# Kernel optimization log

Hardware: AMD Instinct MI355X
Metric: run time of the kernel (lower is better)

Reference implementation:

```python
import jax, jax.numpy as jnp
import numpy as np

INPUT_DIM = 1024
OUTPUT_DIM = 1000
DEPTH = 10
LAMBDA_REG = 1e-3
N_INTERNAL = 2 ** DEPTH - 1
N_LEAF = 2 ** DEPTH
BATCH = 16384


def setup_inputs() -> dict:
    key = jax.random.key(0)
    k1, k2, k3 = jax.random.split(key, 3)
    X = jax.random.normal(k1, (BATCH, INPUT_DIM), dtype=jnp.float32)
    # torch nn.Linear weight layout: [out_features, in_features]; scaled to keep
    # sigmoid routing probs away from 0/1 saturation (log-reg term).
    W_internal = jax.random.normal(k2, (N_INTERNAL, INPUT_DIM + 1), dtype=jnp.float32) * 0.02
    W_leaf = jax.random.normal(k3, (OUTPUT_DIM, N_LEAF), dtype=jnp.float32) * 0.02
    return {"X": X, "W_internal": W_internal, "W_leaf": W_leaf}


def _tree_paths(X, W_internal):
    B = X.shape[0]
    Xb = jnp.concatenate([jnp.ones((B, 1), X.dtype), X], axis=1)  # [B, D+1]
    logits = jax.nn.sigmoid(Xb @ W_internal.T)                    # [B, N_int]
    routing = jnp.stack([logits, 1.0 - logits], axis=2)           # [B, N_int, 2]
    path = jnp.ones((B, 1), X.dtype)
    reg = jnp.float32(0.0)
    start = 0
    for layer in range(DEPTH):
        n = 2 ** layer
        lp = routing[:, start:start + n, :].reshape(B, 2 * n)     # next_paths [B, 2n]
        path = jnp.repeat(path, 2, axis=1) * lp                   # new path probs [B, 2n]
        # Faithful to source: parent_idx = node_idx // 2 indexes the UPDATED path probs.
        parent = jnp.repeat(path[:, :n], 2, axis=1)               # [B, 2n]
        num = jnp.sum(lp * parent, axis=0)                        # [2n]
        den = jnp.sum(parent, axis=0) + 1e-8                      # [2n]
        alpha = num / den
        factor = LAMBDA_REG * 2.0 ** (-layer)
        reg = reg + factor * jnp.sum(-0.5 * (jnp.log(alpha) + jnp.log(1.0 - alpha)))
        start += n
    return path, reg  # path: [B, 2^DEPTH]


def reference(X, W_internal, W_leaf):
    path_probs, reg = _tree_paths(X, W_internal)
    predictions = path_probs @ W_leaf.T   # [B, output_dim]
    return predictions, reg
```

## Files before the change

### kernel.cpp

```cpp
#include <hip/hip_runtime.h>
#include <hip/hip_bf16.h>

#define B_ROWS 16384
#define K_DIM  1024
#define N_INT  1023
#define N_OUT  1000

using s8vec = __attribute__((ext_vector_type(8))) short;
using f32x4 = __attribute__((ext_vector_type(4))) float;

static const size_t OFF_XB   = 0;
static const size_t OFF_W1   = OFF_XB   + 33554432;
static const size_t OFF_BIAS = OFF_W1   + 2097152;
static const size_t OFF_PROB = OFF_BIAS + 4096;
static const size_t OFF_PATH = OFF_PROB + 33554432;
static const size_t OFF_W2   = OFF_PATH + 33554432;
static const size_t OFF_SG   = OFF_W2   + 2097152;

__device__ __forceinline__ float b2f(ushort u) {
  return __uint_as_float(((unsigned)u) << 16);
}
__device__ __forceinline__ float blo(unsigned u) { return __uint_as_float(u << 16); }
__device__ __forceinline__ float bhi(unsigned u) { return __uint_as_float(u & 0xffff0000u); }
__device__ __forceinline__ ushort f2b(float f) {
  unsigned u = __float_as_uint(f);
  u = u + 0x7FFFu + ((u >> 16) & 1u);
  return (ushort)(u >> 16);
}

__device__ __forceinline__ void load_lds16(const ushort* g, ushort* l) {
  __builtin_amdgcn_global_load_lds((const __attribute__((address_space(1))) void*)g,
                                   (__attribute__((address_space(3))) void*)l,
                                   16, 0, 0);
}

__global__ __launch_bounds__(256) void cvt_all(const float4* __restrict__ X,
                                               ushort4* __restrict__ O,
                                               const float* __restrict__ Wi,
                                               const float* __restrict__ Wl,
                                               ushort* __restrict__ W1,
                                               ushort* __restrict__ W2,
                                               float* __restrict__ bias) {
  const int b = blockIdx.x;
  if (b < 16384) {
    const int i = b * 256 + threadIdx.x;
    const float4 v = X[i];
    ushort4 o;
    o.x = f2b(v.x); o.y = f2b(v.y); o.z = f2b(v.z); o.w = f2b(v.w);
    O[i] = o;
  } else {
    const int idx = (b - 16384) * 256 + threadIdx.x;
    if (idx < (1 << 20)) {
      const int n = idx >> 10, k = idx & 1023;
      const float v = (n < N_INT) ? Wi[n * 1025 + 1 + k] : 0.f;
      W1[idx] = f2b(v);
      if (k == 0) bias[n] = (n < N_INT) ? Wi[n * 1025] : 0.f;
    } else {
      const int j = idx - (1 << 20);
      const int n = j >> 10, k = j & 1023;
      const float v = (n < N_OUT) ? Wl[n * 1024 + k] : 0.f;
      W2[j] = f2b(v);
    }
  }
}

template <int MODE>
__global__ __launch_bounds__(256, 4) void gemm_bt(const ushort* __restrict__ A,
                                                  const ushort* __restrict__ Bm,
                                                  const float* __restrict__ bias,
                                                  void* __restrict__ outp) {
  __shared__ ushort As[2][4096];
  __shared__ ushort Bs[2][4096];
  const int tid = threadIdx.x;
  const int bm = blockIdx.x, bn = blockIdx.y;
  const int lane = tid & 63, wv = tid >> 6;
  const int wm = wv >> 1, wn = wv & 1;
  const int m16 = lane & 15, q = lane >> 4;
  const int qs = q ^ ((m16 >> 1) & 3);

  const int r0 = tid >> 2;
  const int qsw = (tid & 3) ^ ((r0 >> 1) & 3);
  const ushort* aG = A  + (size_t)(bm * 128 + r0) * 1024 + qsw * 8;
  const ushort* bG = Bm + (size_t)(bn * 128 + r0) * 1024 + qsw * 8;

  f32x4 acc[4][4] = {};

#define STAGE(buf, kk) do {                                   \
    load_lds16(aG + (kk), As[buf] + wv * 512);                \
    load_lds16(aG + 65536 + (kk), As[buf] + 2048 + wv * 512); \
    load_lds16(bG + (kk), Bs[buf] + wv * 512);                \
    load_lds16(bG + 65536 + (kk), Bs[buf] + 2048 + wv * 512); \
  } while (0)

#define COMPUTE(cur) do {                                                        \
    s8vec af[4], bfv[4];                                                         \
    _Pragma("unroll")                                                            \
    for (int i = 0; i < 4; ++i)                                                  \
      af[i] = *(const s8vec*)(As[cur] + (wm * 64 + i * 16 + m16) * 32 + qs * 8); \
    _Pragma("unroll")                                                            \
    for (int j = 0; j < 4; ++j)                                                  \
      bfv[j] = *(const s8vec*)(Bs[cur] + (wn * 64 + j * 16 + m16) * 32 + qs * 8);\
    _Pragma("unroll")                                                            \
    for (int i = 0; i < 4; ++i)                                                  \
      _Pragma("unroll")                                                          \
      for (int j = 0; j < 4; ++j)                                                \
        acc[i][j] = __builtin_amdgcn_mfma_f32_16x16x32_bf16(af[i], bfv[j],       \
                                                            acc[i][j], 0, 0, 0);\
  } while (0)

  STAGE(0, 0);
#pragma unroll 1
  for (int k0 = 0; k0 < 992; k0 += 32) {
    const int cur = (k0 >> 5) & 1;
    STAGE(cur ^ 1, k0 + 32);
    asm volatile("s_waitcnt vmcnt(4)\n\ts_barrier" ::: "memory");
    COMPUTE(cur);
    asm volatile("s_barrier" ::: "memory");
  }
  asm volatile("s_waitcnt vmcnt(0)\n\ts_barrier" ::: "memory");
  COMPUTE(1);
#undef STAGE
#undef COMPUTE

  if (MODE == 0) {
    ushort* P = (ushort*)outp;
#pragma unroll
    for (int i = 0; i < 4; ++i)
#pragma unroll
      for (int r = 0; r < 4; ++r) {
        const int gr = bm * 128 + wm * 64 + i * 16 + q * 4 + r;
#pragma unroll
        for (int j = 0; j < 4; ++j) {
          const int gc = bn * 128 + wn * 64 + j * 16 + m16;
          const float z = acc[i][j][r] + bias[gc];
          const float p = 1.f / (1.f + expf(-z));
          if (gc < N_INT) P[(size_t)gr * 1024 + gc + 1] = f2b(p);
        }
      }
  } else {
    float* O = (float*)outp;
#pragma unroll
    for (int i = 0; i < 4; ++i)
#pragma unroll
      for (int r = 0; r < 4; ++r) {
        const int gr = bm * 128 + wm * 64 + i * 16 + q * 4 + r;
#pragma unroll
        for (int j = 0; j < 4; ++j) {
          const int gc = bn * 128 + wn * 64 + j * 16 + m16;
          if (gc < N_OUT) O[(size_t)gr * 1000 + gc] = acc[i][j][r];
        }
      }
  }
}

__global__ __launch_bounds__(256) void tree_kernel(const ushort* __restrict__ probs,
                                                   ushort* __restrict__ path) {
  const int lane = threadIdx.x & 63;
  const int r = blockIdx.x * 4 + (threadIdx.x >> 6);
  const ushort* prow = probs + (size_t)r * 1024;

  const int hh  = (int)prow[lane];
  const ushort p6 = prow[64 + lane];
  const uint   p7 = *(const uint*)(prow + 128 + 2 * lane);
  const uint2  p8 = *(const uint2*)(prow + 256 + 4 * lane);
  const uint4  p9 = *(const uint4*)(prow + 512 + 8 * lane);

  float v = 1.f;
#pragma unroll
  for (int t = 1; t <= 6; ++t) {
    const int ell = t - 1;
    const int e = lane >> (6 - t);
    const float p = b2f((ushort)__shfl(hh, (1 << ell) + (e >> 1)));
    v *= (e & 1) ? (1.f - p) : p;
  }

  float w[16];
  { const float p = b2f(p6); w[1] = v * (1.f - p); w[0] = v * p; }
  {
    const float pA = blo(p7), pB = bhi(p7);
    w[3] = w[1] * (1.f - pB); w[2] = w[1] * pB;
    w[1] = w[0] * (1.f - pA); w[0] = w[0] * pA;
  }
  {
    const float pv[4] = { blo(p8.x), bhi(p8.x), blo(p8.y), bhi(p8.y) };
#pragma unroll
    for (int i = 3; i >= 0; --i) {
      w[2 * i + 1] = w[i] * (1.f - pv[i]);
      w[2 * i]     = w[i] * pv[i];
    }
  }
  {
    const uint pv[4] = { p9.x, p9.y, p9.z, p9.w };
#pragma unroll
    for (int i = 7; i >= 0; --i) {
      const float p = (i & 1) ? bhi(pv[i >> 1]) : blo(pv[i >> 1]);
      w[2 * i + 1] = w[i] * (1.f - p);
      w[2 * i]     = w[i] * p;
    }
  }
  union { ushort u[16]; uint4 q4[2]; } pk;
#pragma unroll
  for (int i = 0; i < 16; ++i) pk.u[i] = f2b(w[i]);
  uint4* dst = (uint4*)(path + (size_t)r * 1024 + lane * 16);
  dst[0] = pk.q4[0];
  dst[1] = pk.q4[1];
}

__global__ __launch_bounds__(256) void accum_kernel(const ushort* __restrict__ probs,
                                                    const ushort* __restrict__ path,
                                                    float* __restrict__ Spart) {
  __shared__ float Ss[2048];
  for (int i = threadIdx.x; i < 2048; i += 256) Ss[i] = 0.f;
  __syncthreads();
  const int lane = threadIdx.x & 63;
  const int ll = lane & 31;
  const int half = lane >> 5;
  const int hb = half << 5;
  const int gw = blockIdx.x * 4 + (threadIdx.x >> 6);

  float a19[16] = {}, a29[16] = {};
  float a18[8]  = {}, a28[8]  = {};
  float a17[4]  = {}, a27[4]  = {};
  float a16[2]  = {}, a26[2]  = {};
  float t1[6] = {}, t2[6] = {};

#pragma unroll
  for (int it = 0; it < 2; ++it) {
    const int r = gw * 4 + it * 2 + half;
    const ushort* prow = probs + (size_t)r * 1024;
    const ushort* wrow = path  + (size_t)r * 1024;

    const int   hlo = (int)prow[ll];
    const float p5  = b2f(prow[32 + ll]);
    union { uint4 q[2]; ushort u[16]; } wl;
    wl.q[0] = *(const uint4*)(wrow + 16 * ll);
    wl.q[1] = *(const uint4*)(wrow + 16 * ll + 8);
    union { uint4 q[2]; ushort u[16]; } j9;
    j9.q[0] = *(const uint4*)(prow + 512 + 16 * ll);
    j9.q[1] = *(const uint4*)(prow + 512 + 16 * ll + 8);
    union { uint4 q; ushort u[8]; } j8;
    j8.q = *(const uint4*)(prow + 256 + 8 * ll);
    union { uint2 q; ushort u[4]; } j7;
    j7.q = *(const uint2*)(prow + 128 + 4 * ll);
    union { uint q; ushort u[2]; } j6;
    j6.q = *(const uint*)(prow + 64 + 2 * ll);

    float w[16];
#pragma unroll
    for (int i = 0; i < 16; ++i) w[i] = b2f(wl.u[i]);
    float L8[8], L7[4], L6[2];
#pragma unroll
    for (int i = 0; i < 8; ++i) L8[i] = w[2 * i] + w[2 * i + 1];
#pragma unroll
    for (int i = 0; i < 4; ++i) L7[i] = L8[2 * i] + L8[2 * i + 1];
    L6[0] = L7[0] + L7[1]; L6[1] = L7[2] + L7[3];
    const float T = L6[0] + L6[1];

#pragma unroll
    for (int i = 0; i < 16; ++i) { a19[i] += w[i];  a29[i] += b2f(j9.u[i]) * w[i]; }
#pragma unroll
    for (int i = 0; i < 8; ++i)  { a18[i] += L8[i]; a28[i] += b2f(j8.u[i]) * L8[i]; }
#pragma unroll
    for (int i = 0; i < 4; ++i)  { a17[i] += L7[i]; a27[i] += b2f(j7.u[i]) * L7[i]; }
#pragma unroll
    for (int i = 0; i < 2; ++i)  { a16[i] += L6[i]; a26[i] += b2f(j6.u[i]) * L6[i]; }

    t1[5] += T; t2[5] += p5 * T;
    const float T1 = T  + __shfl_xor(T, 1);
    const float T2 = T1 + __shfl_xor(T1, 2);
    const float T3 = T2 + __shfl_xor(T2, 4);
    const float T4 = T3 + __shfl_xor(T3, 8);
    const float T5 = T4 + __shfl_xor(T4, 16);
    const float v4 = __shfl(T1, hb | ((2 * ll) & 31));
    const float v3 = __shfl(T2, hb | ((4 * ll) & 31));
    const float v2 = __shfl(T3, hb | ((8 * ll) & 31));
    const float v1 = __shfl(T4, hb | ((16 * ll) & 31));
    const float q4 = b2f((ushort)__shfl(hlo, hb | ((16 + ll) & 31)));
    const float q3 = b2f((ushort)__shfl(hlo, hb | ((8 + ll) & 31)));
    const float q2 = b2f((ushort)__shfl(hlo, hb | ((4 + ll) & 31)));
    const float q1 = b2f((ushort)__shfl(hlo, hb | ((2 + ll) & 31)));
    const float q0 = b2f((ushort)__shfl(hlo, hb | 1));
    if (ll < 16) { t1[4] += v4; t2[4] += q4 * v4; }
    if (ll < 8)  { t1[3] += v3; t2[3] += q3 * v3; }
    if (ll < 4)  { t1[2] += v2; t2[2] += q2 * v2; }
    if (ll < 2)  { t1[1] += v1; t2[1] += q1 * v1; }
    if (ll < 1)  { t1[0] += T5; t2[0] += q0 * T5; }
  }

#pragma unroll
  for (int i = 0; i < 16; ++i) { a19[i] += __shfl_xor(a19[i], 32); a29[i] += __shfl_xor(a29[i], 32); }
#pragma unroll
  for (int i = 0; i < 8; ++i)  { a18[i] += __shfl_xor(a18[i], 32); a28[i] += __shfl_xor(a28[i], 32); }
#pragma unroll
  for (int i = 0; i < 4; ++i)  { a17[i] += __shfl_xor(a17[i], 32); a27[i] += __shfl_xor(a27[i], 32); }
#pragma unroll
  for (int i = 0; i < 2; ++i)  { a16[i] += __shfl_xor(a16[i], 32); a26[i] += __shfl_xor(a26[i], 32); }
#pragma unroll
  for (int i = 0; i < 6; ++i)  { t1[i] += __shfl_xor(t1[i], 32);   t2[i] += __shfl_xor(t2[i], 32); }

  if (lane < 32) {
#pragma unroll
    for (int i = 0; i < 16; ++i) { atomicAdd(&Ss[511 + 16 * ll + i], a19[i]); atomicAdd(&Ss[1535 + 16 * ll + i], a29[i]); }
#pragma unroll
    for (int i = 0; i < 8; ++i)  { atomicAdd(&Ss[255 + 8 * ll + i],  a18[i]); atomicAdd(&Ss[1279 + 8 * ll + i],  a28[i]); }
#pragma unroll
    for (int i = 0; i < 4; ++i)  { atomicAdd(&Ss[127 + 4 * ll + i],  a17[i]); atomicAdd(&Ss[1151 + 4 * ll + i],  a27[i]); }
#pragma unroll
    for (int i = 0; i < 2; ++i)  { atomicAdd(&Ss[63 + 2 * ll + i],   a16[i]); atomicAdd(&Ss[1087 + 2 * ll + i],  a26[i]); }
    atomicAdd(&Ss[31 + ll], t1[5]); atomicAdd(&Ss[1055 + ll], t2[5]);
    if (ll < 16) { atomicAdd(&Ss[15 + ll], t1[4]); atomicAdd(&Ss[1039 + ll], t2[4]); }
    if (ll < 8)  { atomicAdd(&Ss[7 + ll],  t1[3]); atomicAdd(&Ss[1031 + ll], t2[3]); }
    if (ll < 4)  { atomicAdd(&Ss[3 + ll],  t1[2]); atomicAdd(&Ss[1027 + ll], t2[2]); }
    if (ll < 2)  { atomicAdd(&Ss[1 + ll],  t1[1]); atomicAdd(&Ss[1025 + ll], t2[1]); }
    if (ll < 1)  { atomicAdd(&Ss[0],       t1[0]); atomicAdd(&Ss[1024],      t2[0]); }
  }
  __syncthreads();
  float* Sp = Spart + (size_t)blockIdx.x * 2048;
  for (int i = threadIdx.x; i < 2048; i += 256) Sp[i] = Ss[i];
}

__global__ __launch_bounds__(256) void reduce_kernel(const float* __restrict__ Spart,
                                                     float* __restrict__ Sg) {
  const int t = threadIdx.x;
  float acc[8] = {};
  const float* base = Spart + (size_t)blockIdx.x * 32 * 2048;
  for (int b = 0; b < 32; ++b) {
    const float* p = base + (size_t)b * 2048;
#pragma unroll
    for (int k = 0; k < 8; ++k) acc[k] += p[t + 256 * k];
  }
#pragma unroll
  for (int k = 0; k < 8; ++k) {
    const int i = t + 256 * k;
    const int node = i & 1023;
    if (node < 1023) atomicAdd(&Sg[(i < 1024 ? 0 : 2048) + node], acc[k]);
  }
}

__global__ __launch_bounds__(1024) void finalize_kernel(const float* __restrict__ Sg,
                                                        float* __restrict__ outreg) {
  const int tid = threadIdx.x;
  double val = 0.0;
  if (tid < 1023) {
    const int ell = 31 - __clz(tid + 1);
    const double s1 = (double)Sg[tid];
    const double s2 = (double)Sg[2048 + tid];
    const double den = s1 + 1e-8;
    const double a0 = s2 / den;
    const double a1 = (s1 - s2) / den;
    const double f = 1e-3 * (1.0 / (double)(1 << ell));
    val = -0.5 * f * (log(a0) + log(1.0 - a0) + log(a1) + log(1.0 - a1));
  }
#pragma unroll
  for (int o = 32; o > 0; o >>= 1) val += __shfl_down(val, o, 64);
  __shared__ double partd[16];
  if ((tid & 63) == 0) partd[tid >> 6] = val;
  __syncthreads();
  if (tid == 0) {
    double t = 0.0;
    for (int i = 0; i < 16; ++i) t += partd[i];
    outreg[0] = (float)t;
  }
}

extern "C" void kernel_launch(void* const* d_in, const int* in_sizes, int n_in,
                              void* d_out, int out_size, void* d_ws, size_t ws_size,
                              hipStream_t stream) {
  const float* X     = (const float*)d_in[0];
  const float* Wint  = (const float*)d_in[1];
  const float* Wleaf = (const float*)d_in[2];
  float* out = (float*)d_out;
  char* ws = (char*)d_ws;

  ushort* Xb   = (ushort*)(ws + OFF_XB);
  ushort* W1   = (ushort*)(ws + OFF_W1);
  float*  bias = (float*)(ws + OFF_BIAS);
  ushort* prob = (ushort*)(ws + OFF_PROB);
  ushort* path = (ushort*)(ws + OFF_PATH);
  ushort* W2   = (ushort*)(ws + OFF_W2);
  float*  Sg   = (float*)(ws + OFF_SG);
  float*  Spart = (float*)(ws + OFF_XB);

  (void)hipMemsetAsync(ws + OFF_SG, 0, 16384, stream);
  cvt_all<<<24576, 256, 0, stream>>>((const float4*)X, (ushort4*)Xb,
                                     Wint, Wleaf, W1, W2, bias);
  gemm_bt<0><<<dim3(128, 8), 256, 0, stream>>>(Xb, W1, bias, (void*)prob);
  tree_kernel<<<4096, 256, 0, stream>>>(prob, path);
  gemm_bt<1><<<dim3(128, 8), 256, 0, stream>>>(path, W2, nullptr, (void*)out);
  accum_kernel<<<1024, 256, 0, stream>>>(prob, path, Spart);
  reduce_kernel<<<32, 256, 0, stream>>>(Spart, Sg);
  finalize_kernel<<<1, 1024, 0, stream>>>(Sg, out + (size_t)B_ROWS * N_OUT);
}
```

Baseline: 308.3 us.

## Fuse tree path computation with regularizer accumulation into one kernel

Merges tree_kernel and accum_kernel so each wave computes path probabilities for four rows, writes them, and accumulates the regularizer statistics from registers. This avoids re-reading the path and prob buffers and drops one launch. The node probabilities the accumulator needs are regathered with lane shuffles. The GEMM also raises occupancy to 5 blocks per CU and uses a fast exp plus hardware reciprocal in the sigmoid epilogue, which risks register spills and slightly lower precision.

Result: faster. 295.9 us (-4.0%).

```diff
diff --git a/kernel.cpp b/kernel.cpp
--- a/kernel.cpp
+++ b/kernel.cpp
@@ -65,7 +65,7 @@
 }
 
 template <int MODE>
-__global__ __launch_bounds__(256, 4) void gemm_bt(const ushort* __restrict__ A,
+__global__ __launch_bounds__(256, 5) void gemm_bt(const ushort* __restrict__ A,
                                                   const ushort* __restrict__ Bm,
                                                   const float* __restrict__ bias,
                                                   void* __restrict__ outp) {
@@ -133,7 +133,7 @@
         for (int j = 0; j < 4; ++j) {
           const int gc = bn * 128 + wn * 64 + j * 16 + m16;
           const float z = acc[i][j][r] + bias[gc];
-          const float p = 1.f / (1.f + expf(-z));
+          const float p = __builtin_amdgcn_rcpf(1.f + __expf(-z));
           if (gc < N_INT) P[(size_t)gr * 1024 + gc + 1] = f2b(p);
         }
       }
@@ -154,68 +154,12 @@
 }
 
 __global__ __launch_bounds__(256) void tree_kernel(const ushort* __restrict__ probs,
-                                                   ushort* __restrict__ path) {
-  const int lane = threadIdx.x & 63;
-  const int r = blockIdx.x * 4 + (threadIdx.x >> 6);
-  const ushort* prow = probs + (size_t)r * 1024;
-
-  const int hh  = (int)prow[lane];
-  const ushort p6 = prow[64 + lane];
-  const uint   p7 = *(const uint*)(prow + 128 + 2 * lane);
-  const uint2  p8 = *(const uint2*)(prow + 256 + 4 * lane);
-  const uint4  p9 = *(const uint4*)(prow + 512 + 8 * lane);
-
-  float v = 1.f;
-#pragma unroll
-  for (int t = 1; t <= 6; ++t) {
-    const int ell = t - 1;
-    const int e = lane >> (6 - t);
-    const float p = b2f((ushort)__shfl(hh, (1 << ell) + (e >> 1)));
-    v *= (e & 1) ? (1.f - p) : p;
-  }
-
-  float w[16];
-  { const float p = b2f(p6); w[1] = v * (1.f - p); w[0] = v * p; }
-  {
-    const float pA = blo(p7), pB = bhi(p7);
-    w[3] = w[1] * (1.f - pB); w[2] = w[1] * pB;
-    w[1] = w[0] * (1.f - pA); w[0] = w[0] * pA;
-  }
-  {
-    const float pv[4] = { blo(p8.x), bhi(p8.x), blo(p8.y), bhi(p8.y) };
-#pragma unroll
-    for (int i = 3; i >= 0; --i) {
-      w[2 * i + 1] = w[i] * (1.f - pv[i]);
-      w[2 * i]     = w[i] * pv[i];
-    }
-  }
-  {
-    const uint pv[4] = { p9.x, p9.y, p9.z, p9.w };
-#pragma unroll
-    for (int i = 7; i >= 0; --i) {
-      const float p = (i & 1) ? bhi(pv[i >> 1]) : blo(pv[i >> 1]);
-      w[2 * i + 1] = w[i] * (1.f - p);
-      w[2 * i]     = w[i] * p;
-    }
-  }
-  union { ushort u[16]; uint4 q4[2]; } pk;
-#pragma unroll
-  for (int i = 0; i < 16; ++i) pk.u[i] = f2b(w[i]);
-  uint4* dst = (uint4*)(path + (size_t)r * 1024 + lane * 16);
-  dst[0] = pk.q4[0];
-  dst[1] = pk.q4[1];
-}
-
-__global__ __launch_bounds__(256) void accum_kernel(const ushort* __restrict__ probs,
-                                                    const ushort* __restrict__ path,
-                                                    float* __restrict__ Spart) {
+                                                   ushort* __restrict__ path,
+                                                   float* __restrict__ Spart) {
   __shared__ float Ss[2048];
   for (int i = threadIdx.x; i < 2048; i += 256) Ss[i] = 0.f;
   __syncthreads();
   const int lane = threadIdx.x & 63;
-  const int ll = lane & 31;
-  const int half = lane >> 5;
-  const int hb = half << 5;
   const int gw = blockIdx.x * 4 + (threadIdx.x >> 6);
 
   float a19[16] = {}, a29[16] = {};
@@ -224,30 +168,56 @@
   float a16[2]  = {}, a26[2]  = {};
   float t1[6] = {}, t2[6] = {};
 
-#pragma unroll
-  for (int it = 0; it < 2; ++it) {
-    const int r = gw * 4 + it * 2 + half;
+#pragma unroll 1
+  for (int rr = 0; rr < 4; ++rr) {
+    const int r = gw * 4 + rr;
     const ushort* prow = probs + (size_t)r * 1024;
-    const ushort* wrow = path  + (size_t)r * 1024;
-
-    const int   hlo = (int)prow[ll];
-    const float p5  = b2f(prow[32 + ll]);
-    union { uint4 q[2]; ushort u[16]; } wl;
-    wl.q[0] = *(const uint4*)(wrow + 16 * ll);
-    wl.q[1] = *(const uint4*)(wrow + 16 * ll + 8);
-    union { uint4 q[2]; ushort u[16]; } j9;
-    j9.q[0] = *(const uint4*)(prow + 512 + 16 * ll);
-    j9.q[1] = *(const uint4*)(prow + 512 + 16 * ll + 8);
-    union { uint4 q; ushort u[8]; } j8;
-    j8.q = *(const uint4*)(prow + 256 + 8 * ll);
-    union { uint2 q; ushort u[4]; } j7;
-    j7.q = *(const uint2*)(prow + 128 + 4 * ll);
-    union { uint q; ushort u[2]; } j6;
-    j6.q = *(const uint*)(prow + 64 + 2 * ll);
-
+
+    const int hh  = (int)prow[lane];
+    const ushort p6 = prow[64 + lane];
+    const uint   p7 = *(const uint*)(prow + 128 + 2 * lane);
+    const uint2  p8 = *(const uint2*)(prow + 256 + 4 * lane);
+    const uint4  p9 = *(const uint4*)(prow + 512 + 8 * lane);
+
+    float v = 1.f;
+#pragma unroll
+    for (int t = 1; t <= 6; ++t) {
+      const int ell = t - 1;
+      const int e = lane >> (6 - t);
+      const float p = b2f((ushort)__shfl(hh, (1 << ell) + (e >> 1)));
+      v *= (e & 1) ? (1.f - p) : p;
+    }
     float w[16];
-#pragma unroll
-    for (int i = 0; i < 16; ++i) w[i] = b2f(wl.u[i]);
+    { const float p = b2f(p6); w[1] = v * (1.f - p); w[0] = v * p; }
+    {
+      const float pA = blo(p7), pB = bhi(p7);
+      w[3] = w[1] * (1.f - pB); w[2] = w[1] * pB;
+      w[1] = w[0] * (1.f - pA); w[0] = w[0] * pA;
+    }
+    {
+      const float pv[4] = { blo(p8.x), bhi(p8.x), blo(p8.y), bhi(p8.y) };
+#pragma unroll
+      for (int i = 3; i >= 0; --i) {
+        w[2 * i + 1] = w[i] * (1.f - pv[i]);
+        w[2 * i]     = w[i] * pv[i];
+      }
+    }
+    {
+      const uint pv[4] = { p9.x, p9.y, p9.z, p9.w };
+#pragma unroll
+      for (int i = 7; i >= 0; --i) {
+        const float p = (i & 1) ? bhi(pv[i >> 1]) : blo(pv[i >> 1]);
+        w[2 * i + 1] = w[i] * (1.f - p);
+        w[2 * i]     = w[i] * p;
+      }
+    }
+    union { ushort u[16]; uint4 q4[2]; } pk;
+#pragma unroll
+    for (int i = 0; i < 16; ++i) pk.u[i] = f2b(w[i]);
+    uint4* dst = (uint4*)(path + (size_t)r * 1024 + lane * 16);
+    dst[0] = pk.q4[0];
+    dst[1] = pk.q4[1];
+
     float L8[8], L7[4], L6[2];
 #pragma unroll
     for (int i = 0; i < 8; ++i) L8[i] = w[2 * i] + w[2 * i + 1];
@@ -256,63 +226,85 @@
     L6[0] = L7[0] + L7[1]; L6[1] = L7[2] + L7[3];
     const float T = L6[0] + L6[1];
 
-#pragma unroll
-    for (int i = 0; i < 16; ++i) { a19[i] += w[i];  a29[i] += b2f(j9.u[i]) * w[i]; }
-#pragma unroll
-    for (int i = 0; i < 8; ++i)  { a18[i] += L8[i]; a28[i] += b2f(j8.u[i]) * L8[i]; }
-#pragma unroll
-    for (int i = 0; i < 4; ++i)  { a17[i] += L7[i]; a27[i] += b2f(j7.u[i]) * L7[i]; }
-#pragma unroll
-    for (int i = 0; i < 2; ++i)  { a16[i] += L6[i]; a26[i] += b2f(j6.u[i]) * L6[i]; }
-
-    t1[5] += T; t2[5] += p5 * T;
+    uint s9[8];
+    s9[0] = (uint)__shfl((int)p9.x, (2 * lane) & 63);
+    s9[1] = (uint)__shfl((int)p9.y, (2 * lane) & 63);
+    s9[2] = (uint)__shfl((int)p9.z, (2 * lane) & 63);
+    s9[3] = (uint)__shfl((int)p9.w, (2 * lane) & 63);
+    s9[4] = (uint)__shfl((int)p9.x, (2 * lane + 1) & 63);
+    s9[5] = (uint)__shfl((int)p9.y, (2 * lane + 1) & 63);
+    s9[6] = (uint)__shfl((int)p9.z, (2 * lane + 1) & 63);
+    s9[7] = (uint)__shfl((int)p9.w, (2 * lane + 1) & 63);
+    const uint u80 = (uint)__shfl((int)p8.x, (2 * lane) & 63);
+    const uint u81 = (uint)__shfl((int)p8.y, (2 * lane) & 63);
+    const uint u82 = (uint)__shfl((int)p8.x, (2 * lane + 1) & 63);
+    const uint u83 = (uint)__shfl((int)p8.y, (2 * lane + 1) & 63);
+    const uint ua7 = (uint)__shfl((int)p7, (2 * lane) & 63);
+    const uint ub7 = (uint)__shfl((int)p7, (2 * lane + 1) & 63);
+    const int  j60 = __shfl((int)p6, (2 * lane) & 63);
+    const int  j61 = __shfl((int)p6, (2 * lane + 1) & 63);
+    if (lane < 32) {
+#pragma unroll
+      for (int i = 0; i < 16; ++i) {
+        const uint u = s9[i >> 1];
+        const float pj = (i & 1) ? bhi(u) : blo(u);
+        a19[i] += w[i]; a29[i] += pj * w[i];
+      }
+      a18[0] += L8[0]; a28[0] += blo(u80) * L8[0];
+      a18[1] += L8[1]; a28[1] += bhi(u80) * L8[1];
+      a18[2] += L8[2]; a28[2] += blo(u81) * L8[2];
+      a18[3] += L8[3]; a28[3] += bhi(u81) * L8[3];
+      a18[4] += L8[4]; a28[4] += blo(u82) * L8[4];
+      a18[5] += L8[5]; a28[5] += bhi(u82) * L8[5];
+      a18[6] += L8[6]; a28[6] += blo(u83) * L8[6];
+      a18[7] += L8[7]; a28[7] += bhi(u83) * L8[7];
+      a17[0] += L7[0]; a27[0] += blo(ua7) * L7[0];
+      a17[1] += L7[1]; a27[1] += bhi(ua7) * L7[1];
+      a17[2] += L7[2]; a27[2] += blo(ub7) * L7[2];
+      a17[3] += L7[3]; a27[3] += bhi(ub7) * L7[3];
+      a16[0] += L6[0]; a26[0] += b2f((ushort)j60) * L6[0];
+      a16[1] += L6[1]; a26[1] += b2f((ushort)j61) * L6[1];
+    }
+
     const float T1 = T  + __shfl_xor(T, 1);
     const float T2 = T1 + __shfl_xor(T1, 2);
     const float T3 = T2 + __shfl_xor(T2, 4);
     const float T4 = T3 + __shfl_xor(T3, 8);
     const float T5 = T4 + __shfl_xor(T4, 16);
-    const float v4 = __shfl(T1, hb | ((2 * ll) & 31));
-    const float v3 = __shfl(T2, hb | ((4 * ll) & 31));
-    const float v2 = __shfl(T3, hb | ((8 * ll) & 31));
-    const float v1 = __shfl(T4, hb | ((16 * ll) & 31));
-    const float q4 = b2f((ushort)__shfl(hlo, hb | ((16 + ll) & 31)));
-    const float q3 = b2f((ushort)__shfl(hlo, hb | ((8 + ll) & 31)));
-    const float q2 = b2f((ushort)__shfl(hlo, hb | ((4 + ll) & 31)));
-    const float q1 = b2f((ushort)__shfl(hlo, hb | ((2 + ll) & 31)));
-    const float q0 = b2f((ushort)__shfl(hlo, hb | 1));
-    if (ll < 16) { t1[4] += v4; t2[4] += q4 * v4; }
-    if (ll < 8)  { t1[3] += v3; t2[3] += q3 * v3; }
-    if (ll < 4)  { t1[2] += v2; t2[2] += q2 * v2; }
-    if (ll < 2)  { t1[1] += v1; t2[1] += q1 * v1; }
-    if (ll < 1)  { t1[0] += T5; t2[0] += q0 * T5; }
-  }
-
-#pragma unroll
-  for (int i = 0; i < 16; ++i) { a19[i] += __shfl_xor(a19[i], 32); a29[i] += __shfl_xor(a29[i], 32); }
-#pragma unroll
-  for (int i = 0; i < 8; ++i)  { a18[i] += __shfl_xor(a18[i], 32); a28[i] += __shfl_xor(a28[i], 32); }
-#pragma unroll
-  for (int i = 0; i < 4; ++i)  { a17[i] += __shfl_xor(a17[i], 32); a27[i] += __shfl_xor(a27[i], 32); }
-#pragma unroll
-  for (int i = 0; i < 2; ++i)  { a16[i] += __shfl_xor(a16[i], 32); a26[i] += __shfl_xor(a26[i], 32); }
-#pragma unroll
-  for (int i = 0; i < 6; ++i)  { t1[i] += __shfl_xor(t1[i], 32);   t2[i] += __shfl_xor(t2[i], 32); }
+    const float v4 = __shfl(T1, (2 * lane) & 63);
+    const float v3 = __shfl(T2, (4 * lane) & 63);
+    const float v2 = __shfl(T3, (8 * lane) & 63);
+    const float v1 = __shfl(T4, (16 * lane) & 63);
+    const float v0 = __shfl(T5, 0);
+    const float q5 = b2f((ushort)__shfl(hh, (32 + lane) & 63));
+    const float q4 = b2f((ushort)__shfl(hh, (16 + lane) & 63));
+    const float q3 = b2f((ushort)__shfl(hh, (8 + lane) & 63));
+    const float q2 = b2f((ushort)__shfl(hh, (4 + lane) & 63));
+    const float q1 = b2f((ushort)__shfl(hh, (2 + lane) & 63));
+    const float q0 = b2f((ushort)__shfl(hh, 1));
+    if (lane < 32) { t1[5] += T;  t2[5] += q5 * T; }
+    if (lane < 16) { t1[4] += v4; t2[4] += q4 * v4; }
+    if (lane < 8)  { t1[3] += v3; t2[3] += q3 * v3; }
+    if (lane < 4)  { t1[2] += v2; t2[2] += q2 * v2; }
+    if (lane < 2)  { t1[1] += v1; t2[1] += q1 * v1; }
+    if (lane < 1)  { t1[0] += v0; t2[0] += q0 * v0; }
+  }
 
   if (lane < 32) {
 #pragma unroll
-    for (int i = 0; i < 16; ++i) { atomicAdd(&Ss[511 + 16 * ll + i], a19[i]); atomicAdd(&Ss[1535 + 16 * ll + i], a29[i]); }
-#pragma unroll
-    for (int i = 0; i < 8; ++i)  { atomicAdd(&Ss[255 + 8 * ll + i],  a18[i]); atomicAdd(&Ss[1279 + 8 * ll + i],  a28[i]); }
-#pragma unroll
-    for (int i = 0; i < 4; ++i)  { atomicAdd(&Ss[127 + 4 * ll + i],  a17[i]); atomicAdd(&Ss[1151 + 4 * ll + i],  a27[i]); }
-#pragma unroll
-    for (int i = 0; i < 2; ++i)  { atomicAdd(&Ss[63 + 2 * ll + i],   a16[i]); atomicAdd(&Ss[1087 + 2 * ll + i],  a26[i]); }
-    atomicAdd(&Ss[31 + ll], t1[5]); atomicAdd(&Ss[1055 + ll], t2[5]);
-    if (ll < 16) { atomicAdd(&Ss[15 + ll], t1[4]); atomicAdd(&Ss[1039 + ll], t2[4]); }
-    if (ll < 8)  { atomicAdd(&Ss[7 + ll],  t1[3]); atomicAdd(&Ss[1031 + ll], t2[3]); }
-    if (ll < 4)  { atomicAdd(&Ss[3 + ll],  t1[2]); atomicAdd(&Ss[1027 + ll], t2[2]); }
-    if (ll < 2)  { atomicAdd(&Ss[1 + ll],  t1[1]); atomicAdd(&Ss[1025 + ll], t2[1]); }
-    if (ll < 1)  { atomicAdd(&Ss[0],       t1[0]); atomicAdd(&Ss[1024],      t2[0]); }
+    for (int i = 0; i < 16; ++i) { atomicAdd(&Ss[511 + 16 * lane + i], a19[i]); atomicAdd(&Ss[1535 + 16 * lane + i], a29[i]); }
+#pragma unroll
+    for (int i = 0; i < 8; ++i)  { atomicAdd(&Ss[255 + 8 * lane + i],  a18[i]); atomicAdd(&Ss[1279 + 8 * lane + i],  a28[i]); }
+#pragma unroll
+    for (int i = 0; i < 4; ++i)  { atomicAdd(&Ss[127 + 4 * lane + i],  a17[i]); atomicAdd(&Ss[1151 + 4 * lane + i],  a27[i]); }
+#pragma unroll
+    for (int i = 0; i < 2; ++i)  { atomicAdd(&Ss[63 + 2 * lane + i],   a16[i]); atomicAdd(&Ss[1087 + 2 * lane + i],  a26[i]); }
+    atomicAdd(&Ss[31 + lane], t1[5]); atomicAdd(&Ss[1055 + lane], t2[5]);
+    if (lane < 16) { atomicAdd(&Ss[15 + lane], t1[4]); atomicAdd(&Ss[1039 + lane], t2[4]); }
+    if (lane < 8)  { atomicAdd(&Ss[7 + lane],  t1[3]); atomicAdd(&Ss[1031 + lane], t2[3]); }
+    if (lane < 4)  { atomicAdd(&Ss[3 + lane],  t1[2]); atomicAdd(&Ss[1027 + lane], t2[2]); }
+    if (lane < 2)  { atomicAdd(&Ss[1 + lane],  t1[1]); atomicAdd(&Ss[1025 + lane], t2[1]); }
+    if (lane < 1)  { atomicAdd(&Ss[0],         t1[0]); atomicAdd(&Ss[1024],        t2[0]); }
   }
   __syncthreads();
   float* Sp = Spart + (size_t)blockIdx.x * 2048;
@@ -385,9 +377,8 @@
   cvt_all<<<24576, 256, 0, stream>>>((const float4*)X, (ushort4*)Xb,
                                      Wint, Wleaf, W1, W2, bias);
   gemm_bt<0><<<dim3(128, 8), 256, 0, stream>>>(Xb, W1, bias, (void*)prob);
-  tree_kernel<<<4096, 256, 0, stream>>>(prob, path);
+  tree_kernel<<<1024, 256, 0, stream>>>(prob, path, Spart);
   gemm_bt<1><<<dim3(128, 8), 256, 0, stream>>>(path, W2, nullptr, (void*)out);
-  accum_kernel<<<1024, 256, 0, stream>>>(prob, path, Spart);
   reduce_kernel<<<32, 256, 0, stream>>>(Spart, Sg);
   finalize_kernel<<<1, 1024, 0, stream>>>(Sg, out + (size_t)B_ROWS * N_OUT);
 }
```
